# Kernel optimization log

Measured on AMD Instinct MI355X. Metric: run time of the kernel, lower is better.

## Reference

```python
import jax, jax.numpy as jnp
import numpy as np

NUM_HEADS = 8  # attention_head_size = C // NUM_HEADS, used only for score scaling


def conv1x1(x, w, b):
    # x: [B, Cin, H, W], w: [Cout, Cin], b: [Cout]
    return jnp.einsum('bchw,oc->bohw', x, w) + b[None, :, None, None]


def setup_inputs() -> dict:
    key = jax.random.key(0)
    ks = jax.random.split(key, 10)
    B, C, H, W = 8, 256, 96, 96
    x = jax.random.normal(ks[0], (B, C, H, W), dtype=jnp.float32)
    y = jax.random.normal(ks[1], (B, 1, 24, 24), dtype=jnp.float32)
    s = 0.02
    wy = jax.random.normal(ks[2], (C, 1), dtype=jnp.float32) * s
    by = jnp.zeros((C,), dtype=jnp.float32)
    wq = jax.random.normal(ks[3], (C, C), dtype=jnp.float32) * s
    bq = jnp.zeros((C,), dtype=jnp.float32)
    wk = jax.random.normal(ks[4], (C, C), dtype=jnp.float32) * s
    bk = jnp.zeros((C,), dtype=jnp.float32)
    wv = jax.random.normal(ks[5], (C, C), dtype=jnp.float32) * s
    bv = jnp.zeros((C,), dtype=jnp.float32)
    return {'x': x, 'y': y, 'wy': wy, 'by': by, 'wq': wq, 'bq': bq,
            'wk': wk, 'bk': bk, 'wv': wv, 'bv': bv}


def reference(x, y, wy, by, wq, bq, wk, bk, wv, bv):
    B, C, H, W = x.shape
    head_size = C // NUM_HEADS
    # x branch
    xq = conv1x1(x, wq, bq)
    xk = conv1x1(x, wk, bk)
    v = conv1x1(x, wv, bv)
    # y branch: 1 -> C channels, bilinear upsample (align_corners=False == half-pixel)
    y2 = conv1x1(y, wy, by)
    y2 = jax.image.resize(y2, (B, C, H, W), method='bilinear')
    yq = conv1x1(y2, wq, bq)
    yk = conv1x1(y2, wk, bk)
    # gated Q/K
    q = (xq * yq).transpose(0, 2, 1, 3)  # [B, H, C, W]
    k = (xk * yk).transpose(0, 2, 1, 3)
    vt = v.transpose(0, 2, 1, 3)
    # channel attention per spatial row: scores [B, H, C, C]
    scores = jnp.einsum('bhcw,bhdw->bhcd', q, k) / jnp.sqrt(jnp.asarray(head_size, x.dtype))
    probs = jax.nn.softmax(scores, axis=-1)
    out = jnp.einsum('bhcd,bhdw->bhcw', probs, vt)
    return out.transpose(0, 2, 1, 3)  # [B, C, H, W]
```

## Files before the change

### kernel.cpp

```cpp
#include <hip/hip_runtime.h>

typedef __bf16 bf16;
typedef __attribute__((ext_vector_type(8))) __bf16 bf16x8;
typedef __attribute__((ext_vector_type(4))) __bf16 bf16x4;
typedef __attribute__((ext_vector_type(4))) float f32x4;

#define MFMA16(A, B, C) __builtin_amdgcn_mfma_f32_16x16x32_bf16(A, B, C, 0, 0, 0)

__global__ __launch_bounds__(256) void k_prep(
    const float* __restrict__ y, const float* __restrict__ wy, const float* __restrict__ by,
    const float* __restrict__ wq, const float* __restrict__ bq,
    const float* __restrict__ wk, const float* __restrict__ bk,
    const float* __restrict__ wv,
    bf16* __restrict__ wq_bf, bf16* __restrict__ wk_bf, bf16* __restrict__ wv_bf,
    float* __restrict__ yu, float* __restrict__ aq, float* __restrict__ cq,
    float* __restrict__ ak, float* __restrict__ ck)
{
  int blk = blockIdx.x, t = threadIdx.x;
  if (blk < 96) {
#pragma unroll
    for (int rep = 0; rep < 2; ++rep) {
      int idx4 = rep * 24576 + blk * 256 + t;
      int fo = idx4 * 4;
      const float* src; bf16* dst; int off;
      if (fo < 65536)       { src = wq; dst = wq_bf; off = fo; }
      else if (fo < 131072) { src = wk; dst = wk_bf; off = fo - 65536; }
      else                  { src = wv; dst = wv_bf; off = fo - 131072; }
      float4 v = *(const float4*)(src + off);
      bf16x4 o;
      o[0] = (bf16)v.x; o[1] = (bf16)v.y; o[2] = (bf16)v.z; o[3] = (bf16)v.w;
      *(bf16x4*)(dst + off) = o;
    }
  } else if (blk < 192) {
    int blkc = blk - 96;
    int b = blkc / 12, seg = blkc % 12;
    const float* yb = y + b * 576;
#pragma unroll
    for (int i = 0; i < 3; ++i) {
      int e = seg * 768 + i * 256 + t;
      int oh = e / 96, ow = e % 96;
      float sh = oh * 0.25f - 0.375f;
      float sw = ow * 0.25f - 0.375f;
      int ih0 = (int)floorf(sh);
      int iw0 = (int)floorf(sw);
      float fh = sh - (float)ih0, fw = sw - (float)iw0;
      int ih0c = min(23, max(0, ih0)), ih1c = min(23, max(0, ih0 + 1));
      int iw0c = min(23, max(0, iw0)), iw1c = min(23, max(0, iw0 + 1));
      float v00 = yb[ih0c * 24 + iw0c], v01 = yb[ih0c * 24 + iw1c];
      float v10 = yb[ih1c * 24 + iw0c], v11 = yb[ih1c * 24 + iw1c];
      yu[b * 9216 + e] = (1.0f - fh) * ((1.0f - fw) * v00 + fw * v01)
                       + fh * ((1.0f - fw) * v10 + fw * v11);
    }
  } else {
    int ol = t >> 5, cl = t & 31;
    int o = (blk - 192) * 8 + ol;
    int c0 = cl * 8;
    float4 wy0 = *(const float4*)(wy + c0), wy1 = *(const float4*)(wy + c0 + 4);
    float4 by0 = *(const float4*)(by + c0), by1 = *(const float4*)(by + c0 + 4);
    float4 q0  = *(const float4*)(wq + o * 256 + c0), q1 = *(const float4*)(wq + o * 256 + c0 + 4);
    float4 k0  = *(const float4*)(wk + o * 256 + c0), k1 = *(const float4*)(wk + o * 256 + c0 + 4);
    float wyv[8] = {wy0.x, wy0.y, wy0.z, wy0.w, wy1.x, wy1.y, wy1.z, wy1.w};
    float byv[8] = {by0.x, by0.y, by0.z, by0.w, by1.x, by1.y, by1.z, by1.w};
    float qv[8]  = {q0.x, q0.y, q0.z, q0.w, q1.x, q1.y, q1.z, q1.w};
    float kv[8]  = {k0.x, k0.y, k0.z, k0.w, k1.x, k1.y, k1.z, k1.w};
    float saq = 0.f, scq = 0.f, sak = 0.f, sck = 0.f;
#pragma unroll
    for (int j = 0; j < 8; ++j) {
      saq += qv[j] * wyv[j]; scq += qv[j] * byv[j];
      sak += kv[j] * wyv[j]; sck += kv[j] * byv[j];
    }
#pragma unroll
    for (int s = 16; s >= 1; s >>= 1) {
      saq += __shfl_xor(saq, s, 32);
      scq += __shfl_xor(scq, s, 32);
      sak += __shfl_xor(sak, s, 32);
      sck += __shfl_xor(sck, s, 32);
    }
    if (cl == 0) {
      aq[o] = saq; cq[o] = scq + bq[o];
      ak[o] = sak; ck[o] = sck + bk[o];
    }
  }
}

__global__ __launch_bounds__(1024, 1) void k_fused(
    const float* __restrict__ x, const float* __restrict__ yu,
    const bf16* __restrict__ wq_bf, const bf16* __restrict__ wk_bf, const bf16* __restrict__ wv_bf,
    const float* __restrict__ bq, const float* __restrict__ bk, const float* __restrict__ bv,
    const float* __restrict__ aq, const float* __restrict__ cq,
    const float* __restrict__ ak, const float* __restrict__ ck,
    float* __restrict__ out)
{
  __shared__ __align__(16) bf16 xs[96 * 264];
  __shared__ __align__(16) bf16 ks[256 * 104];

  int pl = blockIdx.x;
  int b = pl / 96, h = pl % 96;
  int t = threadIdx.x;
  int wid = t >> 6, lane = t & 63;
  int l15 = lane & 15, g = lane >> 4;
  int otile = wid * 16;
  int s8 = (wid + (wid >> 2)) & 7;

  const float* xrow = x + (size_t)b * 2359296 + (size_t)h * 96;

#pragma unroll
  for (int i = 0; i < 3; ++i) {
    int tsk = i * 1024 + t;
    int w = tsk % 96;
    int c0 = (tsk / 96) * 8;
    float v[8];
#pragma unroll
    for (int j = 0; j < 8; ++j) v[j] = xrow[(size_t)(c0 + j) * 9216 + w];
    bf16x8 o8;
#pragma unroll
    for (int j = 0; j < 8; ++j) o8[j] = (bf16)v[j];
    *(bf16x8*)(xs + w * 264 + c0) = o8;
  }

  size_t wo0 = (size_t)(otile + l15) * 256 + g * 8;
  bf16x8 Bq_c = *(const bf16x8*)(wq_bf + wo0 + s8 * 32);
  bf16x8 Bk_c = *(const bf16x8*)(wk_bf + wo0 + s8 * 32);
  bf16x8 Bv_c = *(const bf16x8*)(wv_bf + wo0 + s8 * 32);

  __syncthreads();

  const float SC = 0.17677669529663687f;

  bf16x8 qf[3];

  {
    f32x4 qacc[6] = {};
    f32x4 kacc[6] = {};
    f32x4 vacc[6] = {};
#pragma unroll 1
    for (int i = 0; i < 8; ++i) {
      int kq = (s8 + i) & 7;
      bf16x8 Bq_n, Bk_n, Bv_n;
      if (i < 7) {
        size_t wo = wo0 + (size_t)(((s8 + i + 1) & 7) * 32);
        Bq_n = *(const bf16x8*)(wq_bf + wo);
        Bk_n = *(const bf16x8*)(wk_bf + wo);
        Bv_n = *(const bf16x8*)(wv_bf + wo);
      }
      const bf16* xp = xs + kq * 32 + g * 8;
      bf16x8 A[6];
#pragma unroll
      for (int m = 0; m < 6; ++m)
        A[m] = *(const bf16x8*)(xp + (m * 16 + l15) * 264);
#pragma unroll
      for (int m = 0; m < 6; ++m) {
        qacc[m] = MFMA16(A[m], Bq_c, qacc[m]);
        kacc[m] = MFMA16(A[m], Bk_c, kacc[m]);
        vacc[m] = MFMA16(Bv_c, A[m], vacc[m]);
      }
      Bq_c = Bq_n; Bk_c = Bk_n; Bv_c = Bv_n;
    }

    float4 yv[6];
    {
      const float* yr = yu + (size_t)pl * 96;
#pragma unroll
      for (int mt = 0; mt < 6; ++mt)
        yv[mt] = *(const float4*)(yr + mt * 16 + g * 4);
    }
    int o = otile + l15;
    float bqv = bq[o], aq0 = aq[o], cq0 = cq[o];
    float bkv = bk[o], ak0 = ak[o], ck0 = ck[o];

#pragma unroll
    for (int kk = 0; kk < 3; ++kk) {
      bf16x8 qq;
#pragma unroll
      for (int jh = 0; jh < 2; ++jh) {
        int m = 2 * kk + jh;
        float yy[4] = {yv[m].x, yv[m].y, yv[m].z, yv[m].w};
#pragma unroll
        for (int r = 0; r < 4; ++r)
          qq[jh * 4 + r] = (bf16)((qacc[m][r] + bqv) * (yy[r] * aq0 + cq0) * SC);
      }
      qf[kk] = qq;
    }

#pragma unroll
    for (int m = 0; m < 6; ++m) {
      float yy[4] = {yv[m].x, yv[m].y, yv[m].z, yv[m].w};
      bf16x4 pk;
#pragma unroll
      for (int r = 0; r < 4; ++r)
        pk[r] = (bf16)((kacc[m][r] + bkv) * (yy[r] * ak0 + ck0));
      *(bf16x4*)(ks + (size_t)o * 104 + m * 16 + g * 4) = pk;
    }

    float4 bm = *(const float4*)(bv + otile + g * 4);
    float bb[4] = {bm.x, bm.y, bm.z, bm.w};
    __syncthreads();
    bf16* vs = xs;
    int vbase = (otile & ~16) + ((otile >> 2) & 4);
#pragma unroll
    for (int n = 0; n < 6; ++n) {
      bf16x4 pk;
#pragma unroll
      for (int r = 0; r < 4; ++r) pk[r] = (bf16)(vacc[n][r] + bb[r]);
      *(bf16x4*)(vs + (size_t)(n * 16 + l15) * 264 + vbase + g * 8) = pk;
    }
  }
  __syncthreads();

  const bf16* vs = xs;
  f32x4 oacc[6] = {};
  float lp = 0.f;

  auto load_K = [&](int dt, bf16x8* K) {
    const bf16* kp = ks + (size_t)(dt * 32 + l15) * 104 + g * 4;
#pragma unroll
    for (int kk = 0; kk < 3; ++kk)
#pragma unroll
      for (int dn = 0; dn < 2; ++dn) {
        const bf16* p = kp + (size_t)(dn * 16) * 104 + kk * 32;
        bf16x4 lo = *(const bf16x4*)(p);
        bf16x4 hi = *(const bf16x4*)(p + 16);
        K[kk * 2 + dn] = __builtin_shufflevector(lo, hi, 0, 1, 2, 3, 4, 5, 6, 7);
      }
  };

  bf16x8 KA[6], KB[6];
  load_K(s8, KA);

  auto attn_step = [&](int dt, bf16x8* Kc, bf16x8* Kn, bool pf) {
    int d0 = dt * 32;
    if (pf) load_K((dt + 1) & 7, Kn);
    f32x4 s0 = {}, s1 = {};
    __builtin_amdgcn_s_setprio(1);
#pragma unroll
    for (int kk = 0; kk < 3; ++kk) {
      s0 = MFMA16(Kc[kk * 2 + 0], qf[kk], s0);
      s1 = MFMA16(Kc[kk * 2 + 1], qf[kk], s1);
    }
    __builtin_amdgcn_s_setprio(0);
    bf16x8 pa;
#pragma unroll
    for (int r = 0; r < 4; ++r) {
      float e0 = __expf(s0[r]);
      float e1 = __expf(s1[r]);
      lp += e0 + e1;
      pa[r] = (bf16)e0;
      pa[4 + r] = (bf16)e1;
    }
    const bf16* vp = vs + (size_t)l15 * 264 + d0 + g * 8;
    __builtin_amdgcn_s_setprio(1);
#pragma unroll
    for (int n = 0; n < 6; ++n) {
      bf16x8 Bv = *(const bf16x8*)(vp + (size_t)n * 16 * 264);
      oacc[n] = MFMA16(pa, Bv, oacc[n]);
    }
    __builtin_amdgcn_s_setprio(0);
  };

#pragma unroll 1
  for (int i2 = 0; i2 < 4; ++i2) {
    attn_step((s8 + 2 * i2) & 7,     KA, KB, true);
    attn_step((s8 + 2 * i2 + 1) & 7, KB, KA, 2 * i2 + 1 < 7);
  }

  float vsum = lp;
  vsum += __shfl_xor(vsum, 16, 64);
  vsum += __shfl_xor(vsum, 32, 64);
  float inv = 1.0f / vsum;
  float invr[4];
#pragma unroll
  for (int r = 0; r < 4; ++r)
    invr[r] = __shfl(inv, g * 4 + r, 16);

  float* ob = out + (size_t)b * 2359296 + (size_t)h * 96;
#pragma unroll
  for (int n = 0; n < 6; ++n) {
    int w = n * 16 + l15;
#pragma unroll
    for (int r = 0; r < 4; ++r) {
      int o = otile + g * 4 + r;
      ob[(size_t)o * 9216 + w] = oacc[n][r] * invr[r];
    }
  }
}

extern "C" void kernel_launch(void* const* d_in, const int* in_sizes, int n_in,
                              void* d_out, int out_size, void* d_ws, size_t ws_size,
                              hipStream_t stream) {
  const float* x  = (const float*)d_in[0];
  const float* y  = (const float*)d_in[1];
  const float* wy = (const float*)d_in[2];
  const float* by = (const float*)d_in[3];
  const float* wq = (const float*)d_in[4];
  const float* bq = (const float*)d_in[5];
  const float* wk = (const float*)d_in[6];
  const float* bk = (const float*)d_in[7];
  const float* wv = (const float*)d_in[8];
  const float* bv = (const float*)d_in[9];
  float* out = (float*)d_out;

  char* wsb = (char*)d_ws;
  bf16* wq_bf = (bf16*)(wsb);
  bf16* wk_bf = (bf16*)(wsb + 131072);
  bf16* wv_bf = (bf16*)(wsb + 262144);
  float* yu   = (float*)(wsb + 393216);
  float* aq   = (float*)(wsb + 688128);
  float* cq   = (float*)(wsb + 689152);
  float* ak   = (float*)(wsb + 690176);
  float* ck   = (float*)(wsb + 691200);

  hipLaunchKernelGGL(k_prep, dim3(224), dim3(256), 0, stream,
                     y, wy, by, wq, bq, wk, bk, wv,
                     wq_bf, wk_bf, wv_bf, yu, aq, cq, ak, ck);
  hipLaunchKernelGGL(k_fused, dim3(768), dim3(1024), 0, stream,
                     x, yu, wq_bf, wk_bf, wv_bf, bq, bk, bv,
                     aq, cq, ak, ck, out);
}
```

Before: 211.5 us.

## Split attention across wave pairs sharing two query tiles with partial-sum exchange

Each pair of waves now processes two 16-row query tiles instead of one, each wave covering half of the key dimension (128 keys). This reuses each K and V fragment load for two MFMAs and halves the K loop length per wave. Partial output accumulators and softmax denominators are then exchanged through LDS and combined, with each wave writing half the output columns. The cost is extra register pressure from doubled accumulators, two additional LDS exchanges with barriers, and removal of the staggered start offsets that previously spread LDS bank access.

```diff
diff --git a/kernel.cpp b/kernel.cpp
--- a/kernel.cpp
+++ b/kernel.cpp
@@ -91,8 +91,10 @@
     const float* __restrict__ ak, const float* __restrict__ ck,
     float* __restrict__ out)
 {
-  __shared__ __align__(16) bf16 xs[96 * 264];
-  __shared__ __align__(16) bf16 ks[256 * 104];
+  __shared__ __align__(16) bf16 lds_all[96 * 264 + 256 * 104];
+  __shared__ float lpx[16][32];
+  bf16* xs = lds_all;
+  bf16* ks = lds_all + 96 * 264;
 
   int pl = blockIdx.x;
   int b = pl / 96, h = pl % 96;
@@ -100,7 +102,9 @@
   int wid = t >> 6, lane = t & 63;
   int l15 = lane & 15, g = lane >> 4;
   int otile = wid * 16;
-  int s8 = (wid + (wid >> 2)) & 7;
+  int half = wid & 1;
+  int o32 = (wid >> 1) * 32;
+  int dbase = half * 128;
 
   const float* xrow = x + (size_t)b * 2359296 + (size_t)h * 96;
 
@@ -119,26 +123,25 @@
   }
 
   size_t wo0 = (size_t)(otile + l15) * 256 + g * 8;
-  bf16x8 Bq_c = *(const bf16x8*)(wq_bf + wo0 + s8 * 32);
-  bf16x8 Bk_c = *(const bf16x8*)(wk_bf + wo0 + s8 * 32);
-  bf16x8 Bv_c = *(const bf16x8*)(wv_bf + wo0 + s8 * 32);
+  bf16x8 Bq_c = *(const bf16x8*)(wq_bf + wo0);
+  bf16x8 Bk_c = *(const bf16x8*)(wk_bf + wo0);
+  bf16x8 Bv_c = *(const bf16x8*)(wv_bf + wo0);
 
   __syncthreads();
 
   const float SC = 0.17677669529663687f;
 
-  bf16x8 qf[3];
+  bf16x8 qT0[3], qT1[3];
 
   {
     f32x4 qacc[6] = {};
     f32x4 kacc[6] = {};
     f32x4 vacc[6] = {};
 #pragma unroll 1
-    for (int i = 0; i < 8; ++i) {
-      int kq = (s8 + i) & 7;
+    for (int kq = 0; kq < 8; ++kq) {
       bf16x8 Bq_n, Bk_n, Bv_n;
-      if (i < 7) {
-        size_t wo = wo0 + (size_t)(((s8 + i + 1) & 7) * 32);
+      if (kq < 7) {
+        size_t wo = wo0 + (size_t)((kq + 1) * 32);
         Bq_n = *(const bf16x8*)(wq_bf + wo);
         Bk_n = *(const bf16x8*)(wk_bf + wo);
         Bv_n = *(const bf16x8*)(wv_bf + wo);
@@ -168,6 +171,7 @@
     float bqv = bq[o], aq0 = aq[o], cq0 = cq[o];
     float bkv = bk[o], ak0 = ak[o], ck0 = ck[o];
 
+    bf16x8 qf[3];
 #pragma unroll
     for (int kk = 0; kk < 3; ++kk) {
       bf16x8 qq;
@@ -183,6 +187,26 @@
     }
 
 #pragma unroll
+    for (int kk = 0; kk < 3; ++kk)
+      *(bf16x8*)(ks + otile * 104 + kk * 512 + lane * 8) = qf[kk];
+    __syncthreads();
+    bf16x8 qfP[3];
+    {
+      int potile = (wid ^ 1) * 16;
+#pragma unroll
+      for (int kk = 0; kk < 3; ++kk)
+        qfP[kk] = *(const bf16x8*)(ks + potile * 104 + kk * 512 + lane * 8);
+    }
+    __syncthreads();
+    if (half == 0) {
+#pragma unroll
+      for (int kk = 0; kk < 3; ++kk) { qT0[kk] = qf[kk];  qT1[kk] = qfP[kk]; }
+    } else {
+#pragma unroll
+      for (int kk = 0; kk < 3; ++kk) { qT0[kk] = qfP[kk]; qT1[kk] = qf[kk]; }
+    }
+
+#pragma unroll
     for (int m = 0; m < 6; ++m) {
       float yy[4] = {yv[m].x, yv[m].y, yv[m].z, yv[m].w};
       bf16x4 pk;
@@ -194,7 +218,6 @@
 
     float4 bm = *(const float4*)(bv + otile + g * 4);
     float bb[4] = {bm.x, bm.y, bm.z, bm.w};
-    __syncthreads();
     bf16* vs = xs;
     int vbase = (otile & ~16) + ((otile >> 2) & 4);
 #pragma unroll
@@ -208,11 +231,12 @@
   __syncthreads();
 
   const bf16* vs = xs;
-  f32x4 oacc[6] = {};
-  float lp = 0.f;
-
-  auto load_K = [&](int dt, bf16x8* K) {
-    const bf16* kp = ks + (size_t)(dt * 32 + l15) * 104 + g * 4;
+  f32x4 oaT0[6] = {};
+  f32x4 oaT1[6] = {};
+  float lpT0 = 0.f, lpT1 = 0.f;
+
+  auto load_K = [&](int d0, bf16x8* K) {
+    const bf16* kp = ks + (size_t)(d0 + l15) * 104 + g * 4;
 #pragma unroll
     for (int kk = 0; kk < 3; ++kk)
 #pragma unroll
@@ -225,61 +249,88 @@
   };
 
   bf16x8 KA[6], KB[6];
-  load_K(s8, KA);
-
-  auto attn_step = [&](int dt, bf16x8* Kc, bf16x8* Kn, bool pf) {
-    int d0 = dt * 32;
-    if (pf) load_K((dt + 1) & 7, Kn);
-    f32x4 s0 = {}, s1 = {};
+  load_K(dbase, KA);
+
+  auto attn_step = [&](int d0, bf16x8* Kc, bf16x8* Kn, bool pf) {
+    if (pf) load_K(d0 + 32, Kn);
+    f32x4 s00 = {}, s01 = {}, s10 = {}, s11 = {};
     __builtin_amdgcn_s_setprio(1);
 #pragma unroll
     for (int kk = 0; kk < 3; ++kk) {
-      s0 = MFMA16(Kc[kk * 2 + 0], qf[kk], s0);
-      s1 = MFMA16(Kc[kk * 2 + 1], qf[kk], s1);
+      s00 = MFMA16(Kc[kk * 2 + 0], qT0[kk], s00);
+      s01 = MFMA16(Kc[kk * 2 + 1], qT0[kk], s01);
+      s10 = MFMA16(Kc[kk * 2 + 0], qT1[kk], s10);
+      s11 = MFMA16(Kc[kk * 2 + 1], qT1[kk], s11);
     }
     __builtin_amdgcn_s_setprio(0);
-    bf16x8 pa;
+    bf16x8 pa0, pa1;
 #pragma unroll
     for (int r = 0; r < 4; ++r) {
-      float e0 = __expf(s0[r]);
-      float e1 = __expf(s1[r]);
-      lp += e0 + e1;
-      pa[r] = (bf16)e0;
-      pa[4 + r] = (bf16)e1;
+      float e00 = __expf(s00[r]), e01 = __expf(s01[r]);
+      float e10 = __expf(s10[r]), e11 = __expf(s11[r]);
+      lpT0 += e00 + e01; lpT1 += e10 + e11;
+      pa0[r] = (bf16)e00; pa0[4 + r] = (bf16)e01;
+      pa1[r] = (bf16)e10; pa1[4 + r] = (bf16)e11;
     }
     const bf16* vp = vs + (size_t)l15 * 264 + d0 + g * 8;
     __builtin_amdgcn_s_setprio(1);
 #pragma unroll
     for (int n = 0; n < 6; ++n) {
       bf16x8 Bv = *(const bf16x8*)(vp + (size_t)n * 16 * 264);
-      oacc[n] = MFMA16(pa, Bv, oacc[n]);
+      oaT0[n] = MFMA16(pa0, Bv, oaT0[n]);
+      oaT1[n] = MFMA16(pa1, Bv, oaT1[n]);
     }
     __builtin_amdgcn_s_setprio(0);
   };
 
-#pragma unroll 1
-  for (int i2 = 0; i2 < 4; ++i2) {
-    attn_step((s8 + 2 * i2) & 7,     KA, KB, true);
-    attn_step((s8 + 2 * i2 + 1) & 7, KB, KA, 2 * i2 + 1 < 7);
-  }
-
-  float vsum = lp;
-  vsum += __shfl_xor(vsum, 16, 64);
-  vsum += __shfl_xor(vsum, 32, 64);
-  float inv = 1.0f / vsum;
-  float invr[4];
-#pragma unroll
-  for (int r = 0; r < 4; ++r)
-    invr[r] = __shfl(inv, g * 4 + r, 16);
-
+  attn_step(dbase,      KA, KB, true);
+  attn_step(dbase + 32, KB, KA, true);
+  attn_step(dbase + 64, KA, KB, true);
+  attn_step(dbase + 96, KB, KA, false);
+
+  float v0 = lpT0, v1 = lpT1;
+  v0 += __shfl_xor(v0, 16, 64); v0 += __shfl_xor(v0, 32, 64);
+  v1 += __shfl_xor(v1, 16, 64); v1 += __shfl_xor(v1, 32, 64);
+
+  __syncthreads();
+  float* xbuf = (float*)lds_all;
+  int nF0 = half ? 0 : 3;
+  int base = wid * 1536 + lane * 4;
+#pragma unroll
+  for (int j = 0; j < 3; ++j) {
+    *(f32x4*)(xbuf + base + j * 256)       = oaT0[nF0 + j];
+    *(f32x4*)(xbuf + base + (3 + j) * 256) = oaT1[nF0 + j];
+  }
+  if (g == 0) { lpx[wid][l15] = v0; lpx[wid][16 + l15] = v1; }
+  __syncthreads();
+  int pw = wid ^ 1;
+  int pbase = pw * 1536 + lane * 4;
+  f32x4 pd0[3], pd1[3];
+#pragma unroll
+  for (int j = 0; j < 3; ++j) {
+    pd0[j] = *(const f32x4*)(xbuf + pbase + j * 256);
+    pd1[j] = *(const f32x4*)(xbuf + pbase + (3 + j) * 256);
+  }
+  float inv0 = 1.0f / (v0 + lpx[pw][l15]);
+  float inv1 = 1.0f / (v1 + lpx[pw][16 + l15]);
+  float ir0[4], ir1[4];
+#pragma unroll
+  for (int r = 0; r < 4; ++r) {
+    ir0[r] = __shfl(inv0, g * 4 + r, 16);
+    ir1[r] = __shfl(inv1, g * 4 + r, 16);
+  }
+
+  int nK0 = half ? 3 : 0;
   float* ob = out + (size_t)b * 2359296 + (size_t)h * 96;
 #pragma unroll
-  for (int n = 0; n < 6; ++n) {
-    int w = n * 16 + l15;
+  for (int j = 0; j < 3; ++j) {
+    int w = (nK0 + j) * 16 + l15;
 #pragma unroll
     for (int r = 0; r < 4; ++r) {
-      int o = otile + g * 4 + r;
-      ob[(size_t)o * 9216 + w] = oacc[n][r] * invr[r];
+      int o0 = o32 + g * 4 + r;
+      int o1 = o32 + 16 + g * 4 + r;
+      ob[(size_t)o0 * 9216 + w] = (oaT0[nK0 + j][r] + pd0[j][r]) * ir0[r];
+      ob[(size_t)o1 * 9216 + w] = (oaT1[nK0 + j][r] + pd1[j][r]) * ir1[r];
     }
   }
 }
```

After: 285.4 us. 34.9% more time.

## Halve block size and give each wave two 16-row output tiles

Applied to the files above, without the earlier changes.

The fused kernel now launches 512 threads per block instead of 1024, and each wave computes two 16-channel output tiles instead of one. This reuses each LDS-loaded A fragment and K fragment across two tiles, which cuts LDS reads per MFMA, and launch bounds now allow two blocks per CU. The staggered s8 start offset that spread LDS bank and weight accesses across waves is removed. Doubled accumulators raise register pressure, and LDS use (~103KB per block) may prevent two blocks from actually co-residing.

```diff
diff --git a/kernel.cpp b/kernel.cpp
--- a/kernel.cpp
+++ b/kernel.cpp
@@ -83,7 +83,7 @@
   }
 }
 
-__global__ __launch_bounds__(1024, 1) void k_fused(
+__global__ __launch_bounds__(512, 2) void k_fused(
     const float* __restrict__ x, const float* __restrict__ yu,
     const bf16* __restrict__ wq_bf, const bf16* __restrict__ wk_bf, const bf16* __restrict__ wv_bf,
     const float* __restrict__ bq, const float* __restrict__ bk, const float* __restrict__ bv,
@@ -99,14 +99,14 @@
   int t = threadIdx.x;
   int wid = t >> 6, lane = t & 63;
   int l15 = lane & 15, g = lane >> 4;
-  int otile = wid * 16;
-  int s8 = (wid + (wid >> 2)) & 7;
+  int ot0 = wid * 32;
+  int ot1 = wid * 32 + 16;
 
   const float* xrow = x + (size_t)b * 2359296 + (size_t)h * 96;
 
 #pragma unroll
-  for (int i = 0; i < 3; ++i) {
-    int tsk = i * 1024 + t;
+  for (int i = 0; i < 6; ++i) {
+    int tsk = i * 512 + t;
     int w = tsk % 96;
     int c0 = (tsk / 96) * 8;
     float v[8];
@@ -118,30 +118,35 @@
     *(bf16x8*)(xs + w * 264 + c0) = o8;
   }
 
-  size_t wo0 = (size_t)(otile + l15) * 256 + g * 8;
-  bf16x8 Bq_c = *(const bf16x8*)(wq_bf + wo0 + s8 * 32);
-  bf16x8 Bk_c = *(const bf16x8*)(wk_bf + wo0 + s8 * 32);
-  bf16x8 Bv_c = *(const bf16x8*)(wv_bf + wo0 + s8 * 32);
+  size_t woA = (size_t)(ot0 + l15) * 256 + g * 8;
+  size_t woB = (size_t)(ot1 + l15) * 256 + g * 8;
+  bf16x8 Bq0c = *(const bf16x8*)(wq_bf + woA);
+  bf16x8 Bk0c = *(const bf16x8*)(wk_bf + woA);
+  bf16x8 Bv0c = *(const bf16x8*)(wv_bf + woA);
+  bf16x8 Bq1c = *(const bf16x8*)(wq_bf + woB);
+  bf16x8 Bk1c = *(const bf16x8*)(wk_bf + woB);
+  bf16x8 Bv1c = *(const bf16x8*)(wv_bf + woB);
 
   __syncthreads();
 
   const float SC = 0.17677669529663687f;
 
-  bf16x8 qf[3];
+  bf16x8 qfA[3], qfB[3];
 
   {
-    f32x4 qacc[6] = {};
-    f32x4 kacc[6] = {};
-    f32x4 vacc[6] = {};
+    f32x4 qa0[6] = {}, ka0[6] = {}, va0[6] = {};
+    f32x4 qa1[6] = {}, ka1[6] = {}, va1[6] = {};
 #pragma unroll 1
-    for (int i = 0; i < 8; ++i) {
-      int kq = (s8 + i) & 7;
-      bf16x8 Bq_n, Bk_n, Bv_n;
-      if (i < 7) {
-        size_t wo = wo0 + (size_t)(((s8 + i + 1) & 7) * 32);
-        Bq_n = *(const bf16x8*)(wq_bf + wo);
-        Bk_n = *(const bf16x8*)(wk_bf + wo);
-        Bv_n = *(const bf16x8*)(wv_bf + wo);
+    for (int kq = 0; kq < 8; ++kq) {
+      bf16x8 Bq0n, Bk0n, Bv0n, Bq1n, Bk1n, Bv1n;
+      if (kq < 7) {
+        size_t a = woA + (kq + 1) * 32, bb2 = woB + (kq + 1) * 32;
+        Bq0n = *(const bf16x8*)(wq_bf + a);
+        Bk0n = *(const bf16x8*)(wk_bf + a);
+        Bv0n = *(const bf16x8*)(wv_bf + a);
+        Bq1n = *(const bf16x8*)(wq_bf + bb2);
+        Bk1n = *(const bf16x8*)(wk_bf + bb2);
+        Bv1n = *(const bf16x8*)(wv_bf + bb2);
       }
       const bf16* xp = xs + kq * 32 + g * 8;
       bf16x8 A[6];
@@ -150,11 +155,15 @@
         A[m] = *(const bf16x8*)(xp + (m * 16 + l15) * 264);
 #pragma unroll
       for (int m = 0; m < 6; ++m) {
-        qacc[m] = MFMA16(A[m], Bq_c, qacc[m]);
-        kacc[m] = MFMA16(A[m], Bk_c, kacc[m]);
-        vacc[m] = MFMA16(Bv_c, A[m], vacc[m]);
-      }
-      Bq_c = Bq_n; Bk_c = Bk_n; Bv_c = Bv_n;
+        qa0[m] = MFMA16(A[m], Bq0c, qa0[m]);
+        ka0[m] = MFMA16(A[m], Bk0c, ka0[m]);
+        va0[m] = MFMA16(Bv0c, A[m], va0[m]);
+        qa1[m] = MFMA16(A[m], Bq1c, qa1[m]);
+        ka1[m] = MFMA16(A[m], Bk1c, ka1[m]);
+        va1[m] = MFMA16(Bv1c, A[m], va1[m]);
+      }
+      Bq0c = Bq0n; Bk0c = Bk0n; Bv0c = Bv0n;
+      Bq1c = Bq1n; Bk1c = Bk1n; Bv1c = Bv1n;
     }
 
     float4 yv[6];
@@ -164,52 +173,69 @@
       for (int mt = 0; mt < 6; ++mt)
         yv[mt] = *(const float4*)(yr + mt * 16 + g * 4);
     }
-    int o = otile + l15;
-    float bqv = bq[o], aq0 = aq[o], cq0 = cq[o];
-    float bkv = bk[o], ak0 = ak[o], ck0 = ck[o];
+
+    int o0 = ot0 + l15, o1 = ot1 + l15;
+    float bq0 = bq[o0], aq0 = aq[o0], cq0 = cq[o0];
+    float bk0 = bk[o0], ak0 = ak[o0], ck0 = ck[o0];
+    float bq1 = bq[o1], aq1 = aq[o1], cq1 = cq[o1];
+    float bk1 = bk[o1], ak1 = ak[o1], ck1 = ck[o1];
 
 #pragma unroll
     for (int kk = 0; kk < 3; ++kk) {
-      bf16x8 qq;
+      bf16x8 qq0, qq1;
 #pragma unroll
       for (int jh = 0; jh < 2; ++jh) {
         int m = 2 * kk + jh;
         float yy[4] = {yv[m].x, yv[m].y, yv[m].z, yv[m].w};
 #pragma unroll
-        for (int r = 0; r < 4; ++r)
-          qq[jh * 4 + r] = (bf16)((qacc[m][r] + bqv) * (yy[r] * aq0 + cq0) * SC);
-      }
-      qf[kk] = qq;
+        for (int r = 0; r < 4; ++r) {
+          qq0[jh * 4 + r] = (bf16)((qa0[m][r] + bq0) * (yy[r] * aq0 + cq0) * SC);
+          qq1[jh * 4 + r] = (bf16)((qa1[m][r] + bq1) * (yy[r] * aq1 + cq1) * SC);
+        }
+      }
+      qfA[kk] = qq0;
+      qfB[kk] = qq1;
     }
 
 #pragma unroll
     for (int m = 0; m < 6; ++m) {
       float yy[4] = {yv[m].x, yv[m].y, yv[m].z, yv[m].w};
-      bf16x4 pk;
-#pragma unroll
-      for (int r = 0; r < 4; ++r)
-        pk[r] = (bf16)((kacc[m][r] + bkv) * (yy[r] * ak0 + ck0));
-      *(bf16x4*)(ks + (size_t)o * 104 + m * 16 + g * 4) = pk;
-    }
-
-    float4 bm = *(const float4*)(bv + otile + g * 4);
-    float bb[4] = {bm.x, bm.y, bm.z, bm.w};
+      bf16x4 pk0, pk1;
+#pragma unroll
+      for (int r = 0; r < 4; ++r) {
+        pk0[r] = (bf16)((ka0[m][r] + bk0) * (yy[r] * ak0 + ck0));
+        pk1[r] = (bf16)((ka1[m][r] + bk1) * (yy[r] * ak1 + ck1));
+      }
+      *(bf16x4*)(ks + (size_t)o0 * 104 + m * 16 + g * 4) = pk0;
+      *(bf16x4*)(ks + (size_t)o1 * 104 + m * 16 + g * 4) = pk1;
+    }
+
+    float4 bm0 = *(const float4*)(bv + ot0 + g * 4);
+    float4 bm1 = *(const float4*)(bv + ot1 + g * 4);
+    float bb0[4] = {bm0.x, bm0.y, bm0.z, bm0.w};
+    float bb1[4] = {bm1.x, bm1.y, bm1.z, bm1.w};
     __syncthreads();
     bf16* vs = xs;
-    int vbase = (otile & ~16) + ((otile >> 2) & 4);
+    int vb0 = (ot0 & ~16) + ((ot0 >> 2) & 4);
+    int vb1 = (ot1 & ~16) + ((ot1 >> 2) & 4);
 #pragma unroll
     for (int n = 0; n < 6; ++n) {
-      bf16x4 pk;
-#pragma unroll
-      for (int r = 0; r < 4; ++r) pk[r] = (bf16)(vacc[n][r] + bb[r]);
-      *(bf16x4*)(vs + (size_t)(n * 16 + l15) * 264 + vbase + g * 8) = pk;
+      bf16x4 pk0, pk1;
+#pragma unroll
+      for (int r = 0; r < 4; ++r) {
+        pk0[r] = (bf16)(va0[n][r] + bb0[r]);
+        pk1[r] = (bf16)(va1[n][r] + bb1[r]);
+      }
+      *(bf16x4*)(vs + (size_t)(n * 16 + l15) * 264 + vb0 + g * 8) = pk0;
+      *(bf16x4*)(vs + (size_t)(n * 16 + l15) * 264 + vb1 + g * 8) = pk1;
     }
   }
   __syncthreads();
 
   const bf16* vs = xs;
-  f32x4 oacc[6] = {};
-  float lp = 0.f;
+  f32x4 oaA[6] = {};
+  f32x4 oaB[6] = {};
+  float lpA = 0.f, lpB = 0.f;
 
   auto load_K = [&](int dt, bf16x8* K) {
     const bf16* kp = ks + (size_t)(dt * 32 + l15) * 104 + g * 4;
@@ -225,52 +251,57 @@
   };
 
   bf16x8 KA[6], KB[6];
-  load_K(s8, KA);
+  load_K(0, KA);
 
   auto attn_step = [&](int dt, bf16x8* Kc, bf16x8* Kn, bool pf) {
     int d0 = dt * 32;
-    if (pf) load_K((dt + 1) & 7, Kn);
-    f32x4 s0 = {}, s1 = {};
+    if (pf) load_K(dt + 1, Kn);
+    f32x4 sA0 = {}, sA1 = {}, sB0 = {}, sB1 = {};
     __builtin_amdgcn_s_setprio(1);
 #pragma unroll
     for (int kk = 0; kk < 3; ++kk) {
-      s0 = MFMA16(Kc[kk * 2 + 0], qf[kk], s0);
-      s1 = MFMA16(Kc[kk * 2 + 1], qf[kk], s1);
+      sA0 = MFMA16(Kc[kk * 2 + 0], qfA[kk], sA0);
+      sA1 = MFMA16(Kc[kk * 2 + 1], qfA[kk], sA1);
+      sB0 = MFMA16(Kc[kk * 2 + 0], qfB[kk], sB0);
+      sB1 = MFMA16(Kc[kk * 2 + 1], qfB[kk], sB1);
     }
     __builtin_amdgcn_s_setprio(0);
-    bf16x8 pa;
+    bf16x8 paA, paB;
 #pragma unroll
     for (int r = 0; r < 4; ++r) {
-      float e0 = __expf(s0[r]);
-      float e1 = __expf(s1[r]);
-      lp += e0 + e1;
-      pa[r] = (bf16)e0;
-      pa[4 + r] = (bf16)e1;
+      float eA0 = __expf(sA0[r]), eA1 = __expf(sA1[r]);
+      float eB0 = __expf(sB0[r]), eB1 = __expf(sB1[r]);
+      lpA += eA0 + eA1; lpB += eB0 + eB1;
+      paA[r] = (bf16)eA0; paA[4 + r] = (bf16)eA1;
+      paB[r] = (bf16)eB0; paB[4 + r] = (bf16)eB1;
     }
     const bf16* vp = vs + (size_t)l15 * 264 + d0 + g * 8;
     __builtin_amdgcn_s_setprio(1);
 #pragma unroll
     for (int n = 0; n < 6; ++n) {
       bf16x8 Bv = *(const bf16x8*)(vp + (size_t)n * 16 * 264);
-      oacc[n] = MFMA16(pa, Bv, oacc[n]);
+      oaA[n] = MFMA16(paA, Bv, oaA[n]);
+      oaB[n] = MFMA16(paB, Bv, oaB[n]);
     }
     __builtin_amdgcn_s_setprio(0);
   };
 
 #pragma unroll 1
   for (int i2 = 0; i2 < 4; ++i2) {
-    attn_step((s8 + 2 * i2) & 7,     KA, KB, true);
-    attn_step((s8 + 2 * i2 + 1) & 7, KB, KA, 2 * i2 + 1 < 7);
-  }
-
-  float vsum = lp;
-  vsum += __shfl_xor(vsum, 16, 64);
-  vsum += __shfl_xor(vsum, 32, 64);
-  float inv = 1.0f / vsum;
-  float invr[4];
-#pragma unroll
-  for (int r = 0; r < 4; ++r)
-    invr[r] = __shfl(inv, g * 4 + r, 16);
+    attn_step(2 * i2,     KA, KB, true);
+    attn_step(2 * i2 + 1, KB, KA, 2 * i2 + 1 < 7);
+  }
+
+  float vA = lpA, vB = lpB;
+  vA += __shfl_xor(vA, 16, 64); vA += __shfl_xor(vA, 32, 64);
+  vB += __shfl_xor(vB, 16, 64); vB += __shfl_xor(vB, 32, 64);
+  float invA = 1.0f / vA, invB = 1.0f / vB;
+  float irA[4], irB[4];
+#pragma unroll
+  for (int r = 0; r < 4; ++r) {
+    irA[r] = __shfl(invA, g * 4 + r, 16);
+    irB[r] = __shfl(invB, g * 4 + r, 16);
+  }
 
   float* ob = out + (size_t)b * 2359296 + (size_t)h * 96;
 #pragma unroll
@@ -278,8 +309,10 @@
     int w = n * 16 + l15;
 #pragma unroll
     for (int r = 0; r < 4; ++r) {
-      int o = otile + g * 4 + r;
-      ob[(size_t)o * 9216 + w] = oacc[n][r] * invr[r];
+      int oA = ot0 + g * 4 + r;
+      int oB = ot1 + g * 4 + r;
+      ob[(size_t)oA * 9216 + w] = oaA[n][r] * irA[r];
+      ob[(size_t)oB * 9216 + w] = oaB[n][r] * irB[r];
     }
   }
 }
@@ -312,7 +345,7 @@
   hipLaunchKernelGGL(k_prep, dim3(224), dim3(256), 0, stream,
                      y, wy, by, wq, bq, wk, bk, wv,
                      wq_bf, wk_bf, wv_bf, yu, aq, cq, ak, ck);
-  hipLaunchKernelGGL(k_fused, dim3(768), dim3(1024), 0, stream,
+  hipLaunchKernelGGL(k_fused, dim3(768), dim3(512), 0, stream,
                      x, yu, wq_bf, wk_bf, wv_bf, bq, bk, bv,
                      aq, cq, ak, ck, out);
 }
```

Result: faster. 202.6 us, median of 2 (-4.2%).
